# Optimization experiments

Hardware: AMD Instinct MI355X
Metric: run time of the kernel (lower is better)

## Reference

```python
import jax, jax.numpy as jnp
import numpy as np

N_NODES = 100000
N_EDGES = 1600000
NFEAT = 128
NHID = 64  # layer widths: NFEAT -> 2*NHID -> NHID


def gcn_conv(x, edge_index, edge_weight, W, b):
    """PyG GCNConv: add self-loops, symmetric D^-1/2 (A+I) D^-1/2 normalization."""
    n = x.shape[0]
    h = x @ W  # [N, out]
    src = edge_index[0]
    dst = edge_index[1]
    # degree at destination including self-loop weight 1
    deg = jax.ops.segment_sum(edge_weight, dst, num_segments=n) + 1.0
    dinv = jax.lax.rsqrt(deg)  # deg >= 1, always finite
    norm = dinv[src] * edge_weight * dinv[dst]  # [E]
    agg = jax.ops.segment_sum(h[src] * norm[:, None], dst, num_segments=n)
    agg = agg + h * (dinv * dinv)[:, None]  # self-loop contribution: 1/deg
    return agg + b


def setup_inputs() -> dict:
    key = jax.random.key(0)
    k1, k2, k3, k4, k5, k6 = jax.random.split(key, 6)
    x = jax.random.normal(k1, (N_NODES, NFEAT), dtype=jnp.float32)
    edge_index = jax.random.randint(k2, (2, N_EDGES), 0, N_NODES, dtype=jnp.int64)
    edge_weight = jnp.ones((N_EDGES,), dtype=jnp.float32)
    # GCNConv weights (glorot-ish scale)
    W1 = jax.random.normal(k3, (NFEAT, 2 * NHID), dtype=jnp.float32) / np.sqrt(NFEAT)
    b1 = jnp.zeros((2 * NHID,), dtype=jnp.float32)
    W2 = jax.random.normal(k4, (2 * NHID, NHID), dtype=jnp.float32) / np.sqrt(2 * NHID)
    b2 = jnp.zeros((NHID,), dtype=jnp.float32)
    return {"x": x, "edge_index": edge_index, "edge_weight": edge_weight,
            "W1": W1, "b1": b1, "W2": W2, "b2": b2}


def reference(x, edge_index, edge_weight, W1, b1, W2, b2):
    # GCN_body forward, eval mode (dropout = identity, use_ln/layer_norm_first = False)
    h = jax.nn.relu(gcn_conv(x, edge_index, edge_weight, W1, b1))
    h = jax.nn.relu(gcn_conv(h, edge_index, edge_weight, W2, b2))
    return h
```

## Files before the change

kernel.cpp:

```cpp
#include <hip/hip_runtime.h>

static constexpr int NN = 100000;
static constexpr int NE = 1600000;
static constexpr int BK = 391;
static constexpr int BCAP = 4864;
static constexpr int NBA = 512;
static constexpr int CHUNK = (NE + NBA - 1) / NBA;

typedef _Float16 f16x8 __attribute__((ext_vector_type(8)));
typedef float f32x4 __attribute__((ext_vector_type(4)));

__global__ __launch_bounds__(256) void binA_kernel(const int* __restrict__ src,
                                                   const int* __restrict__ dst,
                                                   const float* __restrict__ w,
                                                   int* __restrict__ bcursor,
                                                   long long* __restrict__ binned) {
  __shared__ int hist[BK];
  __shared__ int base[BK];
  const int t = threadIdx.x;
  const int e0 = blockIdx.x * CHUNK;
  const int e1 = min(e0 + CHUNK, NE);

  for (int i = t; i < BK; i += 256) hist[i] = 0;
  __syncthreads();
  for (int e = e0 + t; e < e1; e += 256) atomicAdd(&hist[dst[e] >> 8], 1);
  __syncthreads();
  for (int i = t; i < BK; i += 256) {
    int h = hist[i];
    base[i] = (h > 0) ? atomicAdd(&bcursor[i], h) : 0;
    hist[i] = 0;
  }
  __syncthreads();
  for (int e = e0 + t; e < e1; e += 256) {
    int d = dst[e];
    int bkt = d >> 8;
    int slot = atomicAdd(&hist[bkt], 1);
    int p = base[bkt] + slot;
    if (p < BCAP) {
      unsigned lo = (unsigned)src[e] | ((unsigned)(d & 255) << 20);
      unsigned long long ent = ((unsigned long long)__float_as_uint(w[e]) << 32) | lo;
      binned[(size_t)bkt * BCAP + p] = (long long)ent;
    }
  }
}

__global__ __launch_bounds__(256) void buildB_kernel(const int* __restrict__ bcursor,
                                                     long long* __restrict__ binned,
                                                     int2* __restrict__ meta,
                                                     float* __restrict__ dinv) {
  __shared__ long long eb[BCAP];
  __shared__ int cnt[256];
  __shared__ int off[256];
  __shared__ int cur[256];
  __shared__ float degs[256];
  __shared__ int wsum[4];
  const int b = blockIdx.x;
  const int t = threadIdx.x;
  const int m = min(bcursor[b], BCAP);
  long long* gb = binned + (size_t)b * BCAP;

  for (int i = t; i < m; i += 256) eb[i] = gb[i];
  cnt[t] = 0;
  degs[t] = 0.f;
  __syncthreads();

  for (int i = t; i < m; i += 256) {
    unsigned long long v = (unsigned long long)eb[i];
    int dl = (int)((v >> 20) & 255u);
    atomicAdd(&cnt[dl], 1);
    atomicAdd(&degs[dl], __uint_as_float((unsigned)(v >> 32)));
  }
  __syncthreads();

  const int lane = t & 63;
  const int c = cnt[t];
  int incl = c;
#pragma unroll
  for (int d2 = 1; d2 < 64; d2 <<= 1) {
    int v2 = __shfl_up(incl, d2, 64);
    if (lane >= d2) incl += v2;
  }
  if (lane == 63) wsum[t >> 6] = incl;
  __syncthreads();
  int wbase = 0;
#pragma unroll
  for (int ww = 0; ww < 4; ++ww) wbase += (ww < (t >> 6)) ? wsum[ww] : 0;
  const int myoff = wbase + incl - c;
  off[t] = myoff;
  cur[t] = 0;
  __syncthreads();

  for (int i = t; i < m; i += 256) {
    long long v = eb[i];
    int dl = (int)(((unsigned long long)v >> 20) & 255u);
    int slot = atomicAdd(&cur[dl], 1);
    gb[off[dl] + slot] = v;
  }

  const int n = b * 256 + t;
  if (n < NN) {
    meta[n] = make_int2(b * BCAP + myoff, c);
    dinv[n] = rsqrtf(degs[t] + 1.0f);
  }
}

template <int N>
__global__ void wfrag_kernel(const float* __restrict__ W, _Float16* __restrict__ wf) {
  int i = blockIdx.x * blockDim.x + threadIdx.x;
  if (i >= N * 128) return;
  int j = i & 7;
  int l = (i >> 3) & 63;
  int ks = (i >> 9) & 3;
  int t = i >> 11;
  int n = t * 16 + (l & 15);
  int k = ks * 32 + (l >> 4) * 8 + j;
  wf[i] = (_Float16)W[k * N + n];
}

template <int N, typename AT>
__global__ __launch_bounds__(256) void mfma_gemm_kernel(const AT* __restrict__ X,
                                                        const _Float16* __restrict__ wf,
                                                        _Float16* __restrict__ H) {
  constexpr int NT = N / 16;
  const int w = threadIdx.x >> 6;
  const int l = threadIdx.x & 63;
  const int row0 = (blockIdx.x * 4 + w) * 16;
  const int arow = row0 + (l & 15);
  const int kb = (l >> 4) * 8;

  f16x8 a[4];
  if (arow < NN) {
    const AT* xp = X + (size_t)arow * 128 + kb;
#pragma unroll
    for (int ks = 0; ks < 4; ++ks) {
      if constexpr (sizeof(AT) == 4) {
        float4 lo = *(const float4*)(xp + ks * 32);
        float4 hi = *(const float4*)(xp + ks * 32 + 4);
        f16x8 v;
        v[0] = (_Float16)lo.x; v[1] = (_Float16)lo.y;
        v[2] = (_Float16)lo.z; v[3] = (_Float16)lo.w;
        v[4] = (_Float16)hi.x; v[5] = (_Float16)hi.y;
        v[6] = (_Float16)hi.z; v[7] = (_Float16)hi.w;
        a[ks] = v;
      } else {
        a[ks] = *(const f16x8*)(xp + ks * 32);
      }
    }
  } else {
    f16x8 z;
#pragma unroll
    for (int j = 0; j < 8; ++j) z[j] = (_Float16)0.f;
#pragma unroll
    for (int ks = 0; ks < 4; ++ks) a[ks] = z;
  }

  f32x4 acc[NT];
#pragma unroll
  for (int t = 0; t < NT; ++t) acc[t] = {0.f, 0.f, 0.f, 0.f};

  const _Float16* wp = wf + l * 8;
#pragma unroll
  for (int t = 0; t < NT; ++t) {
#pragma unroll
    for (int ks = 0; ks < 4; ++ks) {
      f16x8 b = *(const f16x8*)(wp + (size_t)(t * 4 + ks) * 512);
      acc[t] = __builtin_amdgcn_mfma_f32_16x16x32_f16(a[ks], b, acc[t], 0, 0, 0);
    }
  }

  const int r0 = row0 + (l >> 4) * 4;
  const int c0 = l & 15;
#pragma unroll
  for (int t = 0; t < NT; ++t) {
#pragma unroll
    for (int r = 0; r < 4; ++r) {
      int row = r0 + r;
      if (row < NN) H[(size_t)row * N + t * 16 + c0] = (_Float16)acc[t][r];
    }
  }
}

template <int F, typename OT>
__global__ __launch_bounds__(256) void gather_kernel(
    const int2* __restrict__ meta, const long long* __restrict__ csr,
    const _Float16* __restrict__ H, const float* __restrict__ dinv,
    const float* __restrict__ b, OT* __restrict__ out) {
  constexpr int TPN = F / 8;
  constexpr int NPB = 256 / TPN;
  const int t = threadIdx.x;
  const int node = blockIdx.x * NPB + t / TPN;
  if (node >= NN) return;
  const int f = (t % TPN) * 8;

  const int2 mt = meta[node];
  const int lo = mt.x;
  const int hi = mt.x + mt.y;
  const float di = dinv[node];
  const float sl = di * di;

  f16x8 hs = *(const f16x8*)(H + (size_t)node * F + f);
  float c[8], aA[8], aB[8];
#pragma unroll
  for (int j = 0; j < 8; ++j) {
    c[j] = fmaf((float)hs[j], sl, b[f + j]);
    aA[j] = 0.f;
    aB[j] = 0.f;
  }

  int i = lo;
  for (; i + 1 < hi; i += 2) {
    unsigned long long v0 = (unsigned long long)csr[i];
    unsigned long long v1 = (unsigned long long)csr[i + 1];
    int s0 = (int)(v0 & 0x1FFFFu);
    int s1 = (int)(v1 & 0x1FFFFu);
    float n0 = dinv[s0] * __uint_as_float((unsigned)(v0 >> 32));
    float n1 = dinv[s1] * __uint_as_float((unsigned)(v1 >> 32));
    f16x8 h0 = *(const f16x8*)(H + (size_t)s0 * F + f);
    f16x8 h1 = *(const f16x8*)(H + (size_t)s1 * F + f);
#pragma unroll
    for (int j = 0; j < 8; ++j) {
      aA[j] = fmaf((float)h0[j], n0, aA[j]);
      aB[j] = fmaf((float)h1[j], n1, aB[j]);
    }
  }
  if (i < hi) {
    unsigned long long v0 = (unsigned long long)csr[i];
    int s0 = (int)(v0 & 0x1FFFFu);
    float n0 = dinv[s0] * __uint_as_float((unsigned)(v0 >> 32));
    f16x8 h0 = *(const f16x8*)(H + (size_t)s0 * F + f);
#pragma unroll
    for (int j = 0; j < 8; ++j) aA[j] = fmaf((float)h0[j], n0, aA[j]);
  }

  float o[8];
#pragma unroll
  for (int j = 0; j < 8; ++j) o[j] = fmaxf(fmaf(aA[j] + aB[j], di, c[j]), 0.f);

  if constexpr (sizeof(OT) == 2) {
    f16x8 v;
#pragma unroll
    for (int j = 0; j < 8; ++j) v[j] = (_Float16)o[j];
    *(f16x8*)(out + (size_t)node * F + f) = v;
  } else {
    float4 v0 = make_float4(o[0], o[1], o[2], o[3]);
    float4 v1 = make_float4(o[4], o[5], o[6], o[7]);
    *(float4*)(out + (size_t)node * F + f) = v0;
    *(float4*)(out + (size_t)node * F + f + 4) = v1;
  }
}

extern "C" void kernel_launch(void* const* d_in, const int* in_sizes, int n_in,
                              void* d_out, int out_size, void* d_ws, size_t ws_size,
                              hipStream_t stream) {
  const float* x  = (const float*)d_in[0];
  const int*   ei = (const int*)d_in[1];
  const float* ew = (const float*)d_in[2];
  const float* W1 = (const float*)d_in[3];
  const float* b1 = (const float*)d_in[4];
  const float* W2 = (const float*)d_in[5];
  const float* b2 = (const float*)d_in[6];
  float* out = (float*)d_out;

  const int* src = ei;
  const int* dst = ei + NE;

  float* wsf        = (float*)d_ws;
  int*   bcursor    = (int*)wsf;
  float* dinv       = wsf + 512;
  int2*  meta       = (int2*)(wsf + 512 + NN);
  long long* binned = (long long*)(wsf + 512 + 3 * NN);
  float* fbase      = wsf + 512 + 3 * NN + (size_t)BK * BCAP * 2;
  _Float16* h1      = (_Float16*)fbase;
  _Float16* a1      = (_Float16*)(fbase + (size_t)NN * 64);
  _Float16* wf1     = (_Float16*)(fbase + (size_t)NN * 128);
  _Float16* wf2     = wf1 + 16384;
  _Float16* h2      = h1;

  hipMemsetAsync(bcursor, 0, 512 * sizeof(int), stream);

  binA_kernel<<<NBA, 256, 0, stream>>>(src, dst, ew, bcursor, binned);
  buildB_kernel<<<BK, 256, 0, stream>>>(bcursor, binned, meta, dinv);
  wfrag_kernel<128><<<64, 256, 0, stream>>>(W1, wf1);
  wfrag_kernel<64><<<32, 256, 0, stream>>>(W2, wf2);

  mfma_gemm_kernel<128, float><<<(NN + 63) / 64, 256, 0, stream>>>(x, wf1, h1);
  gather_kernel<128, _Float16><<<(NN * 16 + 255) / 256, 256, 0, stream>>>(meta, binned,
                                                                          h1, dinv, b1, a1);

  mfma_gemm_kernel<64, _Float16><<<(NN + 63) / 64, 256, 0, stream>>>(a1, wf2, h2);
  gather_kernel<64, float><<<(NN * 8 + 255) / 256, 256, 0, stream>>>(meta, binned,
                                                                     h2, dinv, b2, out);
}
```

Before: 201.8 us.

## Split edge binning into histogram/scan/scatter, merge wfrag launches, unroll gather by four

Edge binning no longer uses a memset plus global atomic cursors. It now runs a per-block histogram pass, a per-bucket scan that computes deterministic block offsets, and a scatter pass that uses only shared-memory atomics. The two weight-fragment kernels are merged into one launch. The gather loop is unrolled to four independent accumulators to expose more memory-level parallelism. The cost is an extra read of dst, extra launches, and fewer blocks (128) for the binning passes, which may underfill the GPU.

```diff
diff --git a/kernel.cpp b/kernel.cpp
--- a/kernel.cpp
+++ b/kernel.cpp
@@ -4,47 +4,72 @@
 static constexpr int NE = 1600000;
 static constexpr int BK = 391;
 static constexpr int BCAP = 4864;
-static constexpr int NBA = 512;
-static constexpr int CHUNK = (NE + NBA - 1) / NBA;
+static constexpr int NBA = 128;
+static constexpr int CHUNK = NE / NBA;
 
 typedef _Float16 f16x8 __attribute__((ext_vector_type(8)));
 typedef float f32x4 __attribute__((ext_vector_type(4)));
 
-__global__ __launch_bounds__(256) void binA_kernel(const int* __restrict__ src,
-                                                   const int* __restrict__ dst,
-                                                   const float* __restrict__ w,
-                                                   int* __restrict__ bcursor,
-                                                   long long* __restrict__ binned) {
+__global__ __launch_bounds__(256) void histA_kernel(const int* __restrict__ dst,
+                                                    int* __restrict__ cnts) {
   __shared__ int hist[BK];
-  __shared__ int base[BK];
-  const int t = threadIdx.x;
-  const int e0 = blockIdx.x * CHUNK;
-  const int e1 = min(e0 + CHUNK, NE);
-
+  const int t = threadIdx.x;
+  const int b = blockIdx.x;
+  const int e0 = b * CHUNK;
+  const int e1 = e0 + CHUNK;
   for (int i = t; i < BK; i += 256) hist[i] = 0;
   __syncthreads();
   for (int e = e0 + t; e < e1; e += 256) atomicAdd(&hist[dst[e] >> 8], 1);
   __syncthreads();
-  for (int i = t; i < BK; i += 256) {
-    int h = hist[i];
-    base[i] = (h > 0) ? atomicAdd(&bcursor[i], h) : 0;
-    hist[i] = 0;
-  }
+  for (int i = t; i < BK; i += 256) cnts[i * NBA + b] = hist[i];
+}
+
+__global__ __launch_bounds__(128) void scanB_kernel(const int* __restrict__ cnts,
+                                                    int* __restrict__ blockbase,
+                                                    int* __restrict__ bktcnt) {
+  __shared__ int w0s;
+  const int k = blockIdx.x;
+  const int t = threadIdx.x;
+  const int lane = t & 63;
+  const int c = cnts[k * NBA + t];
+  int incl = c;
+#pragma unroll
+  for (int d = 1; d < 64; d <<= 1) {
+    int v = __shfl_up(incl, d, 64);
+    if (lane >= d) incl += v;
+  }
+  if (t == 63) w0s = incl;
+  __syncthreads();
+  const int excl = incl - c + ((t >= 64) ? w0s : 0);
+  blockbase[k * NBA + t] = k * BCAP + excl;
+  if (t == 127) bktcnt[k] = excl + c;
+}
+
+__global__ __launch_bounds__(256) void scatterC_kernel(const int* __restrict__ src,
+                                                       const int* __restrict__ dst,
+                                                       const float* __restrict__ w,
+                                                       const int* __restrict__ blockbase,
+                                                       long long* __restrict__ binned) {
+  __shared__ int cur[BK];
+  const int t = threadIdx.x;
+  const int b = blockIdx.x;
+  const int e0 = b * CHUNK;
+  const int e1 = e0 + CHUNK;
+  for (int i = t; i < BK; i += 256) cur[i] = blockbase[i * NBA + b];
   __syncthreads();
   for (int e = e0 + t; e < e1; e += 256) {
     int d = dst[e];
     int bkt = d >> 8;
-    int slot = atomicAdd(&hist[bkt], 1);
-    int p = base[bkt] + slot;
-    if (p < BCAP) {
+    int p = atomicAdd(&cur[bkt], 1);
+    if (p < (bkt + 1) * BCAP) {
       unsigned lo = (unsigned)src[e] | ((unsigned)(d & 255) << 20);
       unsigned long long ent = ((unsigned long long)__float_as_uint(w[e]) << 32) | lo;
-      binned[(size_t)bkt * BCAP + p] = (long long)ent;
-    }
-  }
-}
-
-__global__ __launch_bounds__(256) void buildB_kernel(const int* __restrict__ bcursor,
+      binned[p] = (long long)ent;
+    }
+  }
+}
+
+__global__ __launch_bounds__(256) void buildB_kernel(const int* __restrict__ bktcnt,
                                                      long long* __restrict__ binned,
                                                      int2* __restrict__ meta,
                                                      float* __restrict__ dinv) {
@@ -56,7 +81,7 @@
   __shared__ int wsum[4];
   const int b = blockIdx.x;
   const int t = threadIdx.x;
-  const int m = min(bcursor[b], BCAP);
+  const int m = min(bktcnt[b], BCAP);
   long long* gb = binned + (size_t)b * BCAP;
 
   for (int i = t; i < m; i += 256) eb[i] = gb[i];
@@ -104,17 +129,24 @@
   }
 }
 
-template <int N>
-__global__ void wfrag_kernel(const float* __restrict__ W, _Float16* __restrict__ wf) {
+__global__ void wfrag_kernel(const float* __restrict__ W1, const float* __restrict__ W2,
+                             _Float16* __restrict__ wf1, _Float16* __restrict__ wf2) {
   int i = blockIdx.x * blockDim.x + threadIdx.x;
-  if (i >= N * 128) return;
-  int j = i & 7;
-  int l = (i >> 3) & 63;
-  int ks = (i >> 9) & 3;
-  int t = i >> 11;
+  const float* W;
+  _Float16* wf;
+  int N, idx;
+  if (i < 128 * 128) {
+    W = W1; wf = wf1; N = 128; idx = i;
+  } else if (i < 128 * 128 + 64 * 128) {
+    W = W2; wf = wf2; N = 64; idx = i - 128 * 128;
+  } else return;
+  int j = idx & 7;
+  int l = (idx >> 3) & 63;
+  int ks = (idx >> 9) & 3;
+  int t = idx >> 11;
   int n = t * 16 + (l & 15);
   int k = ks * 32 + (l >> 4) * 8 + j;
-  wf[i] = (_Float16)W[k * N + n];
+  wf[idx] = (_Float16)W[k * N + n];
 }
 
 template <int N, typename AT>
@@ -199,31 +231,40 @@
   const float sl = di * di;
 
   f16x8 hs = *(const f16x8*)(H + (size_t)node * F + f);
-  float c[8], aA[8], aB[8];
+  float c[8], aA[8], aB[8], aC[8], aD[8];
 #pragma unroll
   for (int j = 0; j < 8; ++j) {
     c[j] = fmaf((float)hs[j], sl, b[f + j]);
-    aA[j] = 0.f;
-    aB[j] = 0.f;
+    aA[j] = 0.f; aB[j] = 0.f; aC[j] = 0.f; aD[j] = 0.f;
   }
 
   int i = lo;
-  for (; i + 1 < hi; i += 2) {
+  for (; i + 3 < hi; i += 4) {
     unsigned long long v0 = (unsigned long long)csr[i];
     unsigned long long v1 = (unsigned long long)csr[i + 1];
+    unsigned long long v2 = (unsigned long long)csr[i + 2];
+    unsigned long long v3 = (unsigned long long)csr[i + 3];
     int s0 = (int)(v0 & 0x1FFFFu);
     int s1 = (int)(v1 & 0x1FFFFu);
+    int s2 = (int)(v2 & 0x1FFFFu);
+    int s3 = (int)(v3 & 0x1FFFFu);
     float n0 = dinv[s0] * __uint_as_float((unsigned)(v0 >> 32));
     float n1 = dinv[s1] * __uint_as_float((unsigned)(v1 >> 32));
+    float n2 = dinv[s2] * __uint_as_float((unsigned)(v2 >> 32));
+    float n3 = dinv[s3] * __uint_as_float((unsigned)(v3 >> 32));
     f16x8 h0 = *(const f16x8*)(H + (size_t)s0 * F + f);
     f16x8 h1 = *(const f16x8*)(H + (size_t)s1 * F + f);
+    f16x8 h2 = *(const f16x8*)(H + (size_t)s2 * F + f);
+    f16x8 h3 = *(const f16x8*)(H + (size_t)s3 * F + f);
 #pragma unroll
     for (int j = 0; j < 8; ++j) {
       aA[j] = fmaf((float)h0[j], n0, aA[j]);
       aB[j] = fmaf((float)h1[j], n1, aB[j]);
-    }
-  }
-  if (i < hi) {
+      aC[j] = fmaf((float)h2[j], n2, aC[j]);
+      aD[j] = fmaf((float)h3[j], n3, aD[j]);
+    }
+  }
+  for (; i < hi; ++i) {
     unsigned long long v0 = (unsigned long long)csr[i];
     int s0 = (int)(v0 & 0x1FFFFu);
     float n0 = dinv[s0] * __uint_as_float((unsigned)(v0 >> 32));
@@ -234,7 +275,8 @@
 
   float o[8];
 #pragma unroll
-  for (int j = 0; j < 8; ++j) o[j] = fmaxf(fmaf(aA[j] + aB[j], di, c[j]), 0.f);
+  for (int j = 0; j < 8; ++j)
+    o[j] = fmaxf(fmaf((aA[j] + aB[j]) + (aC[j] + aD[j]), di, c[j]), 0.f);
 
   if constexpr (sizeof(OT) == 2) {
     f16x8 v;
@@ -265,23 +307,24 @@
   const int* dst = ei + NE;
 
   float* wsf        = (float*)d_ws;
-  int*   bcursor    = (int*)wsf;
-  float* dinv       = wsf + 512;
-  int2*  meta       = (int2*)(wsf + 512 + NN);
-  long long* binned = (long long*)(wsf + 512 + 3 * NN);
-  float* fbase      = wsf + 512 + 3 * NN + (size_t)BK * BCAP * 2;
+  int*   cnts       = (int*)wsf;
+  int*   blockbase  = cnts + BK * NBA;
+  int*   bktcnt     = blockbase + BK * NBA;
+  float* dinv       = (float*)(bktcnt + 512);
+  int2*  meta       = (int2*)(dinv + NN);
+  long long* binned = (long long*)(meta + NN);
+  float* fbase      = (float*)(binned + (size_t)BK * BCAP);
   _Float16* h1      = (_Float16*)fbase;
   _Float16* a1      = (_Float16*)(fbase + (size_t)NN * 64);
   _Float16* wf1     = (_Float16*)(fbase + (size_t)NN * 128);
   _Float16* wf2     = wf1 + 16384;
   _Float16* h2      = h1;
 
-  hipMemsetAsync(bcursor, 0, 512 * sizeof(int), stream);
-
-  binA_kernel<<<NBA, 256, 0, stream>>>(src, dst, ew, bcursor, binned);
-  buildB_kernel<<<BK, 256, 0, stream>>>(bcursor, binned, meta, dinv);
-  wfrag_kernel<128><<<64, 256, 0, stream>>>(W1, wf1);
-  wfrag_kernel<64><<<32, 256, 0, stream>>>(W2, wf2);
+  histA_kernel<<<NBA, 256, 0, stream>>>(dst, cnts);
+  scanB_kernel<<<BK, 128, 0, stream>>>(cnts, blockbase, bktcnt);
+  scatterC_kernel<<<NBA, 256, 0, stream>>>(src, dst, ew, blockbase, binned);
+  buildB_kernel<<<BK, 256, 0, stream>>>(bktcnt, binned, meta, dinv);
+  wfrag_kernel<<<96, 256, 0, stream>>>(W1, W2, wf1, wf2);
 
   mfma_gemm_kernel<128, float><<<(NN + 63) / 64, 256, 0, stream>>>(x, wf1, h1);
   gather_kernel<128, _Float16><<<(NN * 16 + 255) / 256, 256, 0, stream>>>(meta, binned,
```

After: 214.3 us. +6.2%, slower.
